# Optimization experiments

Hardware: AMD Instinct MI355X
Metric: run time of the kernel (lower is better)

## Reference

```python
import jax, jax.numpy as jnp
import numpy as np

BN_EPS = 1e-5


def _bn_relu(x, gamma, beta):
    # training-mode BatchNorm1d over (batch, length) per channel; x: [B,C,N]
    mean = jnp.mean(x, axis=(0, 2), keepdims=True)
    var = jnp.var(x, axis=(0, 2), keepdims=True)  # biased, matching torch normalization
    xh = (x - mean) * jax.lax.rsqrt(var + BN_EPS)
    return jax.nn.relu(xh * gamma[None, :, None] + beta[None, :, None])


def setup_inputs() -> dict:
    key = jax.random.key(0)
    ks = jax.random.split(key, 12)
    B, N, S, C1, C2 = 16, 4096, 1024, 256, 256
    C_in = C1 + C2  # 512
    M0, M1 = 256, 256  # mlp channels
    return {
        "xyz1": jax.random.normal(ks[0], (B, 3, N), dtype=jnp.float32),
        "xyz2": jax.random.normal(ks[1], (B, 3, S), dtype=jnp.float32),
        "points1": jax.random.normal(ks[2], (B, C1, N), dtype=jnp.float32),
        "points2": jax.random.normal(ks[3], (B, C2, S), dtype=jnp.float32),
        "w0": jax.random.normal(ks[4], (M0, C_in), dtype=jnp.float32) * 0.02,
        "b0": jnp.zeros((M0,), dtype=jnp.float32),
        "g0": jnp.ones((M0,), dtype=jnp.float32),
        "be0": jnp.zeros((M0,), dtype=jnp.float32),
        "w1": jax.random.normal(ks[5], (M1, M0), dtype=jnp.float32) * 0.02,
        "b1": jnp.zeros((M1,), dtype=jnp.float32),
        "g1": jnp.ones((M1,), dtype=jnp.float32),
        "be1": jnp.zeros((M1,), dtype=jnp.float32),
    }


def reference(xyz1, xyz2, points1, points2, w0, b0, g0, be0, w1, b1, g1, be1):
    # xyz1: [B,3,N], xyz2: [B,3,S], points1: [B,C1,N], points2: [B,C2,S]
    xyz1_t = xyz1.transpose(0, 2, 1)  # [B,N,3]
    xyz2_t = xyz2.transpose(0, 2, 1)  # [B,S,3]
    p2_t = points2.transpose(0, 2, 1)  # [B,S,C2]

    # squared pairwise distances [B,N,S] via |a|^2 + |b|^2 - 2ab
    d = (jnp.sum(xyz1_t ** 2, -1)[:, :, None]
         + jnp.sum(xyz2_t ** 2, -1)[:, None, :]
         - 2.0 * jnp.einsum('bnd,bsd->bns', xyz1_t, xyz2_t))

    # 3 nearest neighbours (smallest distances)
    neg_d3, idx = jax.lax.top_k(-d, 3)  # [B,N,3]
    dists = -neg_d3

    recip = 1.0 / (dists + 1e-8)
    weight = recip / jnp.sum(recip, axis=-1, keepdims=True)  # [B,N,3]

    gathered = jax.vmap(lambda p, i: p[i])(p2_t, idx)  # [B,N,3,C2]
    interp = jnp.sum(gathered * weight[..., None], axis=2)  # [B,N,C2]

    new_points = jnp.concatenate([points1.transpose(0, 2, 1), interp], axis=-1)  # [B,N,C1+C2]
    x = new_points.transpose(0, 2, 1)  # [B,C_in,N]

    # 1x1 Conv1d == per-position matmul
    x = _bn_relu(jnp.einsum('oi,bin->bon', w0, x) + b0[None, :, None], g0, be0)
    x = _bn_relu(jnp.einsum('oi,bin->bon', w1, x) + b1[None, :, None], g1, be1)
    return x
```

## Files before the change

### kernel.cpp

```cpp
#include <hip/hip_runtime.h>
#include <stdint.h>

using u16 = unsigned short;
using short8 = __attribute__((ext_vector_type(8))) short;
using f32x4  = __attribute__((ext_vector_type(4))) float;
using u32x4  = __attribute__((ext_vector_type(4))) unsigned int;

__device__ __forceinline__ float bf2f(u16 u) {
  return __builtin_bit_cast(float, ((unsigned)u) << 16);
}
__device__ __forceinline__ u16 f2bf(float f) {
  unsigned u = __builtin_bit_cast(unsigned, f);
  u += 0x7FFFu + ((u >> 16) & 1u);
  return (u16)(u >> 16);
}

__device__ __forceinline__ void ins3(float& d0, float& d1, float& d2,
                                     int& i0, int& i1, int& i2, float d, int s) {
  bool c0 = d < d0, c1 = d < d1, c2 = d < d2;
  d2 = c1 ? d1 : (c2 ? d : d2);
  i2 = c1 ? i1 : (c2 ? s : i2);
  d1 = c0 ? d0 : (c1 ? d : d1);
  i1 = c0 ? i0 : (c1 ? s : i1);
  d0 = c0 ? d : d0;
  i0 = c0 ? s : i0;
}

__global__ __launch_bounds__(256) void nn3_kernel(
    const float* __restrict__ xyz1, const float* __restrict__ xyz2,
    int* __restrict__ idx_out, float* __restrict__ w_out) {
  __shared__ __align__(16) float cand[1024][4];
  const int b = blockIdx.y;
  const int t = threadIdx.x;
  const float* x2 = xyz2 + b * 3072;
  for (int i = t; i < 1024; i += 256) {
    float x = x2[i], y = x2[1024 + i], z = x2[2048 + i];
    cand[i][0] = x; cand[i][1] = y; cand[i][2] = z;
    cand[i][3] = x*x + y*y + z*z;
  }
  __syncthreads();
  const int q = t >> 2, sub = t & 3;
  const int n = blockIdx.x * 64 + q;
  const float* x1 = xyz1 + b * 12288;
  const float px = x1[n], py = x1[4096 + n], pz = x1[8192 + n];
  const float r1 = px*px + py*py + pz*pz;
  float d0 = 1e30f, d1 = 1e30f, d2 = 1e30f;
  int i0 = 0, i1 = 0, i2 = 0;
  const int sbeg = sub << 8;
  #pragma unroll 4
  for (int s = sbeg; s < sbeg + 256; ++s) {
    f32x4 c = *(const f32x4*)cand[s];
    float dot = px*c[0] + py*c[1] + pz*c[2];
    float d = (r1 + c[3]) - 2.0f*dot;
    ins3(d0, d1, d2, i0, i1, i2, d, s);
  }
  for (int st = 1; st <= 2; st <<= 1) {
    float e0 = __shfl_xor(d0, st), e1 = __shfl_xor(d1, st), e2 = __shfl_xor(d2, st);
    int   j0 = __shfl_xor(i0, st), j1 = __shfl_xor(i1, st), j2 = __shfl_xor(i2, st);
    ins3(d0, d1, d2, i0, i1, i2, e0, j0);
    ins3(d0, d1, d2, i0, i1, i2, e1, j1);
    ins3(d0, d1, d2, i0, i1, i2, e2, j2);
  }
  if (sub == 0) {
    float w0 = 1.0f/(d0 + 1e-8f), w1 = 1.0f/(d1 + 1e-8f), w2 = 1.0f/(d2 + 1e-8f);
    float inv = 1.0f/(w0 + w1 + w2);
    const int pos = b * 4096 + n;
    idx_out[pos*3+0] = i0; idx_out[pos*3+1] = i1; idx_out[pos*3+2] = i2;
    w_out[pos*3+0] = w0*inv; w_out[pos*3+1] = w1*inv; w_out[pos*3+2] = w2*inv;
  }
}

__global__ __launch_bounds__(256) void transpose_cl(
    const float* __restrict__ in, u16* __restrict__ out, int L, int rstride) {
  __shared__ u16 tile[64][66];
  const int b = blockIdx.z;
  in  += (size_t)b * 256 * L;
  out += (size_t)b * L * rstride;
  const int n0 = blockIdx.x * 64, c0 = blockIdx.y * 64;
  const int t = threadIdx.x, ln = t & 63, grp = t >> 6;
  for (int p = 0; p < 16; ++p) {
    int cc = p*4 + grp;
    tile[cc][ln] = f2bf(in[(size_t)(c0 + cc) * L + n0 + ln]);
  }
  __syncthreads();
  for (int p = 0; p < 16; ++p) {
    int nn = p*4 + grp;
    out[(size_t)(n0 + nn) * rstride + c0 + ln] = tile[ln][nn];
  }
}

__global__ __launch_bounds__(256) void cvt_kernel(const float* __restrict__ in,
                                                  u16* __restrict__ out, int n) {
  int i = blockIdx.x * 256 + threadIdx.x;
  if (i < n) out[i] = f2bf(in[i]);
}

__global__ __launch_bounds__(256) void interp_kernel(
    const u16* __restrict__ p2t, const int* __restrict__ idx,
    const float* __restrict__ wgt, u16* __restrict__ A1) {
  const int t = threadIdx.x;
  const int base = blockIdx.x * 16;
  for (int i = 0; i < 16; ++i) {
    const int pos = base + i;
    const int b = pos >> 12;
    const int j0 = idx[pos*3+0], j1 = idx[pos*3+1], j2 = idx[pos*3+2];
    const float w0 = wgt[pos*3+0], w1 = wgt[pos*3+1], w2 = wgt[pos*3+2];
    const u16* r0 = p2t + ((size_t)(b*1024 + j0)) * 256;
    const u16* r1 = p2t + ((size_t)(b*1024 + j1)) * 256;
    const u16* r2 = p2t + ((size_t)(b*1024 + j2)) * 256;
    float v = w0*bf2f(r0[t]) + w1*bf2f(r1[t]) + w2*bf2f(r2[t]);
    A1[(size_t)pos*512 + 256 + t] = f2bf(v);
  }
}

__global__ __launch_bounds__(256) void gemm_kernel(
    const u16* __restrict__ A, const u16* __restrict__ Bw,
    const float* __restrict__ bias, u16* __restrict__ Y, int K) {
  __shared__ __align__(16) u16 As[128*48];
  __shared__ __align__(16) u16 Bs[128*48];
  const int t = threadIdx.x;
  const int m0 = blockIdx.x * 128, n0 = blockIdx.y * 128;
  const int wave = t >> 6, l = t & 63;
  const int wm = wave & 1, wn = wave >> 1;
  const int lc = l & 15, quad = l >> 4;
  f32x4 acc[4][4] = {};
  const int rowA = t >> 2, kc = (t & 3) * 8;
  for (int k0 = 0; k0 < K; k0 += 32) {
    *(u32x4*)&As[rowA*48 + kc]      = *(const u32x4*)&A[(size_t)(m0 + rowA)*K + k0 + kc];
    *(u32x4*)&As[(rowA+64)*48 + kc] = *(const u32x4*)&A[(size_t)(m0 + rowA + 64)*K + k0 + kc];
    *(u32x4*)&Bs[rowA*48 + kc]      = *(const u32x4*)&Bw[(size_t)(n0 + rowA)*K + k0 + kc];
    *(u32x4*)&Bs[(rowA+64)*48 + kc] = *(const u32x4*)&Bw[(size_t)(n0 + rowA + 64)*K + k0 + kc];
    __syncthreads();
    short8 af[4], bfv[4];
    for (int tm = 0; tm < 4; ++tm)
      af[tm] = *(const short8*)&As[(wm*64 + tm*16 + lc)*48 + quad*8];
    for (int tn = 0; tn < 4; ++tn)
      bfv[tn] = *(const short8*)&Bs[(wn*64 + tn*16 + lc)*48 + quad*8];
    for (int tm = 0; tm < 4; ++tm)
      for (int tn = 0; tn < 4; ++tn)
        acc[tm][tn] = __builtin_amdgcn_mfma_f32_16x16x32_bf16(af[tm], bfv[tn], acc[tm][tn], 0, 0, 0);
    __syncthreads();
  }
  for (int tn = 0; tn < 4; ++tn) {
    const int col = n0 + wn*64 + tn*16 + lc;
    const float bb = bias[col];
    for (int tm = 0; tm < 4; ++tm) {
      const int row = m0 + wm*64 + tm*16 + quad*4;
      for (int r = 0; r < 4; ++r)
        Y[(size_t)(row + r)*256 + col] = f2bf(acc[tm][tn][r] + bb);
    }
  }
}

__global__ __launch_bounds__(256) void colstats_kernel(
    const u16* __restrict__ Y, float* __restrict__ sums, float* __restrict__ sumsq) {
  const int t = threadIdx.x;
  size_t base = (size_t)blockIdx.x * 256 * 256;
  float s = 0.0f, q = 0.0f;
  for (int r = 0; r < 256; ++r) {
    float v = bf2f(Y[base + (size_t)r*256 + t]);
    s += v; q += v*v;
  }
  atomicAdd(&sums[t], s);
  atomicAdd(&sumsq[t], q);
}

__global__ void bnprep_kernel(const float* __restrict__ sums, const float* __restrict__ sumsq,
                              const float* __restrict__ g, const float* __restrict__ be,
                              float* __restrict__ scale, float* __restrict__ shift) {
  const int t = threadIdx.x;
  const float inv_n = 1.0f / 65536.0f;
  float mean = sums[t] * inv_n;
  float var = sumsq[t] * inv_n - mean*mean;
  float a = g[t] * rsqrtf(var + 1e-5f);
  scale[t] = a;
  shift[t] = be[t] - mean * a;
}

__global__ __launch_bounds__(256) void bnrelu_kernel(
    const u16* __restrict__ Y, const float* __restrict__ scale,
    const float* __restrict__ shift, u16* __restrict__ X) {
  const int t = threadIdx.x;
  const float a = scale[t], s = shift[t];
  size_t base = (size_t)blockIdx.x * 16 * 256;
  for (int r = 0; r < 16; ++r) {
    float v = bf2f(Y[base + r*256 + t]) * a + s;
    X[base + r*256 + t] = f2bf(v > 0.0f ? v : 0.0f);
  }
}

__global__ __launch_bounds__(256) void bnrelu_tr_kernel(
    const u16* __restrict__ Y, const float* __restrict__ scale,
    const float* __restrict__ shift, float* __restrict__ out) {
  __shared__ u16 tile[256][66];
  const int t = threadIdx.x;
  const int b = blockIdx.z;
  const int n0 = blockIdx.x * 64;
  const float a = scale[t], s = shift[t];
  for (int nn = 0; nn < 64; ++nn) {
    size_t pos = (size_t)b*4096 + n0 + nn;
    float v = bf2f(Y[pos*256 + t]) * a + s;
    tile[t][nn] = f2bf(v > 0.0f ? v : 0.0f);
  }
  __syncthreads();
  const int ln = t & 63, grp = t >> 6;
  for (int p = 0; p < 64; ++p) {
    int oo = p*4 + grp;
    out[((size_t)b*256 + oo)*4096 + n0 + ln] = bf2f(tile[oo][ln]);
  }
}

extern "C" void kernel_launch(void* const* d_in, const int* in_sizes, int n_in,
                              void* d_out, int out_size, void* d_ws, size_t ws_size,
                              hipStream_t stream) {
  const float* xyz1    = (const float*)d_in[0];
  const float* xyz2    = (const float*)d_in[1];
  const float* points1 = (const float*)d_in[2];
  const float* points2 = (const float*)d_in[3];
  const float* w0      = (const float*)d_in[4];
  const float* b0      = (const float*)d_in[5];
  const float* g0      = (const float*)d_in[6];
  const float* be0     = (const float*)d_in[7];
  const float* w1      = (const float*)d_in[8];
  const float* b1      = (const float*)d_in[9];
  const float* g1      = (const float*)d_in[10];
  const float* be1     = (const float*)d_in[11];
  float* out = (float*)d_out;

  char* ws = (char*)d_ws;
  u16*   A1   = (u16*)ws;
  u16*   X0   = (u16*)ws;
  u16*   Y    = (u16*)(ws + (64ull  << 20));
  u16*   p2t  = (u16*)(ws + (96ull  << 20));
  int*   idxb = (int*)(ws + (104ull << 20));
  float* wgtb = (float*)(ws + (105ull << 20));
  u16*   w0b  = (u16*)(ws + (106ull << 20));
  u16*   w1b  = (u16*)(ws + (106ull << 20) + (256u << 10));
  float* stats= (float*)(ws + (106ull << 20) + (512u << 10));

  float* sums0 = stats, *sumsq0 = stats + 256, *scale0 = stats + 512, *shift0 = stats + 768;
  float* sums1 = stats + 1024, *sumsq1 = stats + 1280, *scale1 = stats + 1536, *shift1 = stats + 1792;

  hipMemsetAsync(stats, 0, 2048 * sizeof(float), stream);
  nn3_kernel<<<dim3(64, 16), 256, 0, stream>>>(xyz1, xyz2, idxb, wgtb);
  transpose_cl<<<dim3(16, 4, 16), 256, 0, stream>>>(points2, p2t, 1024, 256);
  transpose_cl<<<dim3(64, 4, 16), 256, 0, stream>>>(points1, A1, 4096, 512);
  cvt_kernel<<<512, 256, 0, stream>>>(w0, w0b, 131072);
  cvt_kernel<<<256, 256, 0, stream>>>(w1, w1b, 65536);
  interp_kernel<<<4096, 256, 0, stream>>>(p2t, idxb, wgtb, A1);
  gemm_kernel<<<dim3(512, 2), 256, 0, stream>>>(A1, w0b, b0, Y, 512);
  colstats_kernel<<<256, 256, 0, stream>>>(Y, sums0, sumsq0);
  bnprep_kernel<<<1, 256, 0, stream>>>(sums0, sumsq0, g0, be0, scale0, shift0);
  bnrelu_kernel<<<4096, 256, 0, stream>>>(Y, scale0, shift0, X0);
  gemm_kernel<<<dim3(512, 2), 256, 0, stream>>>(X0, w1b, b1, Y, 256);
  colstats_kernel<<<256, 256, 0, stream>>>(Y, sums1, sumsq1);
  bnprep_kernel<<<1, 256, 0, stream>>>(sums1, sumsq1, g1, be1, scale1, shift1);
  bnrelu_tr_kernel<<<dim3(64, 1, 16), 256, 0, stream>>>(Y, scale1, shift1, out);
}
```

Before: 331.5 us.

## Fuse BN column statistics into GEMM epilogue and use async global-to-LDS loads

Removes the separate colstats kernels by accumulating per-column sum and sum-of-squares in the GEMM epilogue, with wave shuffles followed by atomics. The statistics now come from fp32 values before bf16 rounding rather than from the stored bf16 output. It also replaces the register-staged tile loads with global_load_lds direct-to-LDS copies and drops the LDS row padding from 48 to 32 elements. The unpadded layout may add LDS bank conflicts, and the GEMM epilogue now issues many more atomics.

```diff
diff --git a/kernel.cpp b/kernel.cpp
--- a/kernel.cpp
+++ b/kernel.cpp
@@ -13,6 +13,12 @@
   unsigned u = __builtin_bit_cast(unsigned, f);
   u += 0x7FFFu + ((u >> 16) & 1u);
   return (u16)(u >> 16);
+}
+
+__device__ __forceinline__ void async_copy16(const u16* g, u16* l) {
+  __builtin_amdgcn_global_load_lds(
+      (const __attribute__((address_space(1))) unsigned int*)g,
+      (__attribute__((address_space(3))) unsigned int*)l, 16, 0, 0);
 }
 
 __device__ __forceinline__ void ins3(float& d0, float& d1, float& d2,
@@ -115,54 +121,58 @@
 
 __global__ __launch_bounds__(256) void gemm_kernel(
     const u16* __restrict__ A, const u16* __restrict__ Bw,
-    const float* __restrict__ bias, u16* __restrict__ Y, int K) {
-  __shared__ __align__(16) u16 As[128*48];
-  __shared__ __align__(16) u16 Bs[128*48];
+    const float* __restrict__ bias, u16* __restrict__ Y, int K,
+    float* __restrict__ sums, float* __restrict__ sumsq) {
+  __shared__ __align__(16) u16 As[128*32];
+  __shared__ __align__(16) u16 Bs[128*32];
   const int t = threadIdx.x;
   const int m0 = blockIdx.x * 128, n0 = blockIdx.y * 128;
-  const int wave = t >> 6, l = t & 63;
-  const int wm = wave & 1, wn = wave >> 1;
+  const int wv = t >> 6, l = t & 63;
+  const int wm = wv & 1, wn = wv >> 1;
   const int lc = l & 15, quad = l >> 4;
   f32x4 acc[4][4] = {};
-  const int rowA = t >> 2, kc = (t & 3) * 8;
+
+  const u16* Ag = A + (size_t)(m0 + (wv << 4) + (l >> 2)) * K + (l & 3) * 8;
+  const u16* Bg = Bw + (size_t)(n0 + (wv << 4) + (l >> 2)) * K + (l & 3) * 8;
+  u16* As0 = As + wv * 512;
+  u16* As1 = As + 2048 + wv * 512;
+  u16* Bs0 = Bs + wv * 512;
+  u16* Bs1 = Bs + 2048 + wv * 512;
+  const size_t rstep = (size_t)64 * K;
+
   for (int k0 = 0; k0 < K; k0 += 32) {
-    *(u32x4*)&As[rowA*48 + kc]      = *(const u32x4*)&A[(size_t)(m0 + rowA)*K + k0 + kc];
-    *(u32x4*)&As[(rowA+64)*48 + kc] = *(const u32x4*)&A[(size_t)(m0 + rowA + 64)*K + k0 + kc];
-    *(u32x4*)&Bs[rowA*48 + kc]      = *(const u32x4*)&Bw[(size_t)(n0 + rowA)*K + k0 + kc];
-    *(u32x4*)&Bs[(rowA+64)*48 + kc] = *(const u32x4*)&Bw[(size_t)(n0 + rowA + 64)*K + k0 + kc];
+    async_copy16(Ag + k0,         As0);
+    async_copy16(Ag + rstep + k0, As1);
+    async_copy16(Bg + k0,         Bs0);
+    async_copy16(Bg + rstep + k0, Bs1);
     __syncthreads();
     short8 af[4], bfv[4];
     for (int tm = 0; tm < 4; ++tm)
-      af[tm] = *(const short8*)&As[(wm*64 + tm*16 + lc)*48 + quad*8];
+      af[tm] = *(const short8*)&As[(wm*64 + tm*16 + lc)*32 + quad*8];
     for (int tn = 0; tn < 4; ++tn)
-      bfv[tn] = *(const short8*)&Bs[(wn*64 + tn*16 + lc)*48 + quad*8];
+      bfv[tn] = *(const short8*)&Bs[(wn*64 + tn*16 + lc)*32 + quad*8];
     for (int tm = 0; tm < 4; ++tm)
       for (int tn = 0; tn < 4; ++tn)
         acc[tm][tn] = __builtin_amdgcn_mfma_f32_16x16x32_bf16(af[tm], bfv[tn], acc[tm][tn], 0, 0, 0);
     __syncthreads();
   }
+
   for (int tn = 0; tn < 4; ++tn) {
     const int col = n0 + wn*64 + tn*16 + lc;
     const float bb = bias[col];
+    float sp = 0.0f, qp = 0.0f;
     for (int tm = 0; tm < 4; ++tm) {
       const int row = m0 + wm*64 + tm*16 + quad*4;
-      for (int r = 0; r < 4; ++r)
-        Y[(size_t)(row + r)*256 + col] = f2bf(acc[tm][tn][r] + bb);
+      for (int r = 0; r < 4; ++r) {
+        float v = acc[tm][tn][r] + bb;
+        Y[(size_t)(row + r)*256 + col] = f2bf(v);
+        sp += v; qp += v*v;
+      }
     }
-  }
-}
-
-__global__ __launch_bounds__(256) void colstats_kernel(
-    const u16* __restrict__ Y, float* __restrict__ sums, float* __restrict__ sumsq) {
-  const int t = threadIdx.x;
-  size_t base = (size_t)blockIdx.x * 256 * 256;
-  float s = 0.0f, q = 0.0f;
-  for (int r = 0; r < 256; ++r) {
-    float v = bf2f(Y[base + (size_t)r*256 + t]);
-    s += v; q += v*v;
-  }
-  atomicAdd(&sums[t], s);
-  atomicAdd(&sumsq[t], q);
+    sp += __shfl_xor(sp, 16); qp += __shfl_xor(qp, 16);
+    sp += __shfl_xor(sp, 32); qp += __shfl_xor(qp, 32);
+    if (quad == 0) { atomicAdd(&sums[col], sp); atomicAdd(&sumsq[col], qp); }
+  }
 }
 
 __global__ void bnprep_kernel(const float* __restrict__ sums, const float* __restrict__ sumsq,
@@ -248,12 +258,10 @@
   cvt_kernel<<<512, 256, 0, stream>>>(w0, w0b, 131072);
   cvt_kernel<<<256, 256, 0, stream>>>(w1, w1b, 65536);
   interp_kernel<<<4096, 256, 0, stream>>>(p2t, idxb, wgtb, A1);
-  gemm_kernel<<<dim3(512, 2), 256, 0, stream>>>(A1, w0b, b0, Y, 512);
-  colstats_kernel<<<256, 256, 0, stream>>>(Y, sums0, sumsq0);
+  gemm_kernel<<<dim3(512, 2), 256, 0, stream>>>(A1, w0b, b0, Y, 512, sums0, sumsq0);
   bnprep_kernel<<<1, 256, 0, stream>>>(sums0, sumsq0, g0, be0, scale0, shift0);
   bnrelu_kernel<<<4096, 256, 0, stream>>>(Y, scale0, shift0, X0);
-  gemm_kernel<<<dim3(512, 2), 256, 0, stream>>>(X0, w1b, b1, Y, 256);
-  colstats_kernel<<<256, 256, 0, stream>>>(Y, sums1, sumsq1);
+  gemm_kernel<<<dim3(512, 2), 256, 0, stream>>>(X0, w1b, b1, Y, 256, sums1, sumsq1);
   bnprep_kernel<<<1, 256, 0, stream>>>(sums1, sumsq1, g1, be1, scale1, shift1);
   bnrelu_tr_kernel<<<dim3(64, 1, 16), 256, 0, stream>>>(Y, scale1, shift1, out);
 }
```

After: 386.1 us. 16.5% more time.
